# Optimization experiments

Hardware: AMD Instinct MI355X
Metric: run time of the kernel (lower is better)

The kernel has to match this reference:

```python
import jax, jax.numpy as jnp
import numpy as np

D = 1024      # hidden_size
FF = 4096     # ff_inner_dim = 4 * D
E = 8         # num_experts
K = 2         # moe_top_k
B, L = 4, 1024


def setup_inputs() -> dict:
    key = jax.random.key(0)
    ks = jax.random.split(key, 12)
    s = 0.02  # weight init scale
    return {
        "x": jax.random.normal(ks[0], (B, L, D), jnp.float32),
        "W_gate": jax.random.normal(ks[1], (D, E), jnp.float32) * s,
        "W1": jax.random.normal(ks[2], (E, D, FF), jnp.float32) * s,
        "b1": jnp.zeros((E, FF), jnp.float32),
        "W2": jax.random.normal(ks[3], (E, FF, D), jnp.float32) * s,
        "b2": jnp.zeros((E, D), jnp.float32),
        "Ws1": jax.random.normal(ks[4], (D, FF), jnp.float32) * s,
        "bs1": jnp.zeros((FF,), jnp.float32),
        "Ws2": jax.random.normal(ks[5], (FF, D), jnp.float32) * s,
        "bs2": jnp.zeros((D,), jnp.float32),
    }


def _gelu(h):
    # torch F.gelu default = exact (erf) gelu
    return jax.nn.gelu(h, approximate=False)


def reference(x, W_gate, W1, b1, W2, b2, Ws1, bs1, Ws2, bs2):
    Bx, Lx, Dx = x.shape
    xf = x.reshape(-1, Dx)                       # [T, D]
    logits = xf @ W_gate                         # [T, E]
    probs = jax.nn.softmax(logits, axis=-1)
    top_v, top_i = jax.lax.top_k(probs, K)       # [T, K]
    top_v = top_v / jnp.sum(top_v, axis=-1, keepdims=True)
    # dense combine weights: [T, E], zero for unselected experts
    combine = jnp.sum(jax.nn.one_hot(top_i, E, dtype=xf.dtype) * top_v[..., None], axis=1)

    out = jnp.zeros_like(xf)
    for e in range(E):  # fixed small expert loop, unrolled under jit
        h = _gelu(xf @ W1[e] + b1[e])            # [T, FF]
        out = out + combine[:, e:e + 1] * (h @ W2[e] + b2[e])

    shared = _gelu(xf @ Ws1 + bs1) @ Ws2 + bs2   # [T, D]
    return (out + shared).reshape(Bx, Lx, Dx)
```

## Files before the change

kernel.cpp:

```cpp
#include <hip/hip_runtime.h>
#include <hip/hip_bf16.h>

typedef unsigned short ushort_t;
typedef __attribute__((ext_vector_type(4))) float f32x4;
typedef __attribute__((ext_vector_type(8))) short bf16x8;
typedef __attribute__((ext_vector_type(8))) unsigned short us8;

#define T_TOK 4096
#define D_DIM 1024
#define FF_DIM 4096
#define NE 8
#define ESTRIDE 4194304L

__device__ __forceinline__ unsigned short f2bf(float f) {
  __hip_bfloat16 h = __float2bfloat16(f);
  return __builtin_bit_cast(unsigned short, h);
}
__device__ __forceinline__ float bf2f(ushort_t u) {
  unsigned int x = ((unsigned int)u) << 16;
  return __builtin_bit_cast(float, x);
}
__device__ __forceinline__ float gelu_f(float v) {
  return 0.5f * v * (1.0f + erff(v * 0.70710678118654752440f));
}

__global__ __launch_bounds__(256) void pre_kernel(
    const float* __restrict__ x, const float* __restrict__ Wg,
    const float* __restrict__ W1, const float* __restrict__ Ws1,
    int* __restrict__ cnt, int* __restrict__ tok,
    float* __restrict__ wof, int* __restrict__ rankof,
    ushort_t* __restrict__ Xbf, ushort_t* __restrict__ W1T) {
  __shared__ ushort_t tile[128][136];
  const int bid = blockIdx.x, tid = threadIdx.x;

  if (bid < 1024) {
    const int t = bid * 4 + (tid >> 6);
    const int lane = tid & 63;
    const float* xr = x + (long)t * D_DIM;
    ushort_t* xb = Xbf + (long)t * D_DIM;
    float acc[NE];
#pragma unroll
    for (int e = 0; e < NE; e++) acc[e] = 0.f;
#pragma unroll
    for (int i = 0; i < 16; i++) {
      int d = i * 64 + lane;
      float xv = xr[d];
      xb[d] = f2bf(xv);
      const float* wr = Wg + d * NE;
#pragma unroll
      for (int e = 0; e < NE; e++) acc[e] += xv * wr[e];
    }
#pragma unroll
    for (int off = 32; off > 0; off >>= 1) {
#pragma unroll
      for (int e = 0; e < NE; e++) acc[e] += __shfl_xor(acc[e], off, 64);
    }
    if (lane == 0) {
      int i0 = 0;
#pragma unroll
      for (int e = 1; e < NE; e++) if (acc[e] > acc[i0]) i0 = e;
      int i1 = -1;
#pragma unroll
      for (int e = 0; e < NE; e++) {
        if (e == i0) continue;
        if (i1 < 0 || acc[e] > acc[i1]) i1 = e;
      }
      float e1 = expf(acc[i1] - acc[i0]);
      float w0 = 1.f / (1.f + e1);
      float w1 = e1 * w0;
      int s0 = atomicAdd(&cnt[i0], 1);
      tok[i0 * T_TOK + s0] = t; wof[i0 * T_TOK + s0] = w0; rankof[i0 * T_TOK + s0] = 0;
      int s1 = atomicAdd(&cnt[i1], 1);
      tok[i1 * T_TOK + s1] = t; wof[i1 * T_TOK + s1] = w1; rankof[i1 * T_TOK + s1] = 1;
      tok[8 * T_TOK + t] = t; wof[8 * T_TOK + t] = 1.f; rankof[8 * T_TOK + t] = 0;
    }
    return;
  }

  int tix = bid - 1024;
  if (tix >= 2304) return;
  const int e = tix >> 8;
  const int rem = tix & 255;
  const int r0 = (rem >> 5) * 128, c0 = (rem & 31) * 128;
  const float* src = (e == 8) ? Ws1 : (W1 + (long)e * 4194304);
  ushort_t* d = W1T + (long)e * ESTRIDE;
#pragma unroll
  for (int i = 0; i < 16; i++) {
    int lin = tid + i * 256;
    int r = lin >> 5, c = (lin & 31) * 4;
    float4 v = *(const float4*)(src + (long)(r0 + r) * 4096 + c0 + c);
    tile[c + 0][r] = f2bf(v.x);
    tile[c + 1][r] = f2bf(v.y);
    tile[c + 2][r] = f2bf(v.z);
    tile[c + 3][r] = f2bf(v.w);
  }
  __syncthreads();
#pragma unroll
  for (int i = 0; i < 8; i++) {
    int lin = tid + i * 256;
    int cc = lin >> 4, rp = lin & 15;
    us8 v = *(const us8*)&tile[cc][rp * 8];
    *(us8*)(d + (long)(c0 + cc) * 1024 + r0 + rp * 8) = v;
  }
}

__global__ void build_queue_kernel(const int* __restrict__ cnt, int* __restrict__ base,
                                   unsigned int* __restrict__ q1,
                                   unsigned int* __restrict__ q2,
                                   int* __restrict__ nq, int* __restrict__ cnt8) {
  const int e = blockIdx.x;
  int off1 = 0, off2 = 0, tot1 = 0, tot2 = 0, M = 0;
  for (int i = 0; i < 9; i++) {
    int c = (i == 8) ? T_TOK : cnt[i];
    int m = (c + 255) >> 8;
    if (i < e) { off1 += m * 16; off2 += m * 4; }
    if (i == e) M = m;
    tot1 += m * 16; tot2 += m * 4;
  }
  for (int i = threadIdx.x; i < M * 16; i += 256) {
    int my = i >> 4, nx = i & 15;
    int ms = my >> 1, mi = my & 1, ns = nx >> 2, ni = nx & 3;
    int h = M - ms * 2; if (h > 2) h = 2;
    int pos = ms * 32 + ns * (h * 4) + mi * 4 + ni;
    q1[off1 + pos] = ((unsigned)e << 16) | ((unsigned)my << 8) | (unsigned)nx;
  }
  for (int i = threadIdx.x; i < M * 4; i += 256) {
    int my = i >> 2, nx = i & 3;
    int pos = nx * M + my;
    q2[off2 + pos] = ((unsigned)e << 16) | ((unsigned)my << 8) | (unsigned)nx;
  }
  if (e == 0 && threadIdx.x == 0) {
    nq[0] = tot1; nq[1] = tot2;
    int s = 0;
    for (int i = 0; i < NE; i++) { base[i] = s; s += cnt[i]; }
    base[8] = s;
    *cnt8 = T_TOK;
  }
}

template <int K, int N, int PHASE, bool FUSE>
__global__ __launch_bounds__(1024, 1) void gemm_kernel(
    const ushort_t* __restrict__ Abase, const ushort_t* __restrict__ WT,
    const float* __restrict__ bias_e, const float* __restrict__ bias_s,
    const int* __restrict__ cnt, const int* __restrict__ base,
    const int* __restrict__ tok, const float* __restrict__ wof,
    const int* __restrict__ rankof,
    const unsigned int* __restrict__ q, const int* __restrict__ nq_all,
    ushort_t* __restrict__ He, ushort_t* __restrict__ ybuf, float* __restrict__ out,
    const float* __restrict__ W2src, const float* __restrict__ Ws2src,
    ushort_t* __restrict__ W2Tdst) {
  __shared__ char smem[131072];
  const int tid = threadIdx.x;
  const int bid = blockIdx.x;
  const int NBLK = FUSE ? 1024 : (int)gridDim.x;

  if (FUSE && bid >= 1024) {
    int tix = bid - 1024;
    if (tix >= 2304) return;
    const int e = tix >> 8;
    const int rem = tix & 255;
    const int r0 = (rem >> 3) * 128, c0 = (rem & 7) * 128;
    const float* src = (e == 8) ? Ws2src : (W2src + (long)e * 4194304);
    ushort_t* d = W2Tdst + (long)e * ESTRIDE;
    ushort_t (*tile)[136] = (ushort_t (*)[136])smem;
#pragma unroll
    for (int i = 0; i < 4; i++) {
      int lin = tid + i * 1024;
      int r = lin >> 5, c = (lin & 31) * 4;
      float4 v = *(const float4*)(src + (long)(r0 + r) * 1024 + c0 + c);
      tile[c + 0][r] = f2bf(v.x);
      tile[c + 1][r] = f2bf(v.y);
      tile[c + 2][r] = f2bf(v.z);
      tile[c + 3][r] = f2bf(v.w);
    }
    __syncthreads();
#pragma unroll
    for (int i = 0; i < 2; i++) {
      int lin = tid + i * 1024;
      int cc = lin >> 4, rp = lin & 15;
      us8 v = *(const us8*)&tile[cc][rp * 8];
      *(us8*)(d + (long)(c0 + cc) * 4096 + r0 + rp * 8) = v;
    }
    return;
  }

  const int nq = nq_all[PHASE - 1];
  const int chunk = NBLK >> 3;
  const int vbid = (bid < (chunk << 3)) ? ((bid & 7) * chunk + (bid >> 3)) : bid;

  const int w = tid >> 6, lane = tid & 63;
  const int wm = w >> 2, wn = w & 3;
  const int lr = lane & 15, lg = lane >> 4;
  char* const lds = smem;

  const int srow = tid >> 2;
  const int cg = ((tid & 3) - (srow >> 1)) & 3;

  int offA[4], offB[4];
#pragma unroll
  for (int m = 0; m < 4; m++) {
    int r = wm * 64 + m * 16 + lr;
    offA[m] = r * 64 + (((lg + (r >> 1)) & 3) << 4);
  }
#pragma unroll
  for (int n = 0; n < 4; n++) {
    int r = wn * 64 + n * 16 + lr;
    offB[n] = r * 64 + (((lg + (r >> 1)) & 3) << 4);
  }

  constexpr int NT = K / 32;

#define STAGE(buf_, kk_)                                                        \
  do {                                                                          \
    char* dd_ = lds + (buf_) * 32768 + tid * 16;                                \
    __builtin_amdgcn_global_load_lds(                                           \
        (const __attribute__((address_space(1))) void*)(pA + (kk_)),            \
        (__attribute__((address_space(3))) void*)(dd_), 16, 0, 0);              \
    __builtin_amdgcn_global_load_lds(                                           \
        (const __attribute__((address_space(1))) void*)(pB + (kk_)),            \
        (__attribute__((address_space(3))) void*)(dd_ + 16384), 16, 0, 0);      \
  } while (0)

  for (int it = vbid; it < nq; it += NBLK) {
    const unsigned int item = q[it];
    const int e = item >> 16;
    const int m0 = ((item >> 8) & 0xff) * 256;
    const int n0 = (item & 0xff) * 256;
    const int count = cnt[e];

    int rr = m0 + srow;
    int rc = (rr < count) ? rr : 0;
    long arow;
    if (PHASE == 1) arow = tok[e * T_TOK + rc];
    else            arow = (long)base[e] + rc;
    const ushort_t* pA = Abase + arow * (long)K + cg * 8;
    const ushort_t* pB = WT + (long)e * ESTRIDE + (long)(n0 + srow) * K + cg * 8;

    f32x4 acc[4][4] = {};

    __builtin_amdgcn_s_barrier();
    asm volatile("" ::: "memory");
    STAGE(0, 0); STAGE(1, 32); STAGE(2, 64);

    for (int t = 0; t < NT; t++) {
      if (t + 3 < NT) {
        STAGE((t + 3) & 3, (t + 3) * 32);
        asm volatile("s_waitcnt vmcnt(6)" ::: "memory");
      } else if (t + 3 == NT) {
        asm volatile("s_waitcnt vmcnt(4)" ::: "memory");
      } else if (t + 2 == NT) {
        asm volatile("s_waitcnt vmcnt(2)" ::: "memory");
      } else {
        asm volatile("s_waitcnt vmcnt(0)" ::: "memory");
      }
      __builtin_amdgcn_s_barrier();
      asm volatile("" ::: "memory");

      const char* aB = lds + (t & 3) * 32768;
      const char* bB = aB + 16384;
      bf16x8 av[4], bv[4];
#pragma unroll
      for (int m = 0; m < 4; m++) av[m] = *(const bf16x8*)(aB + offA[m]);
#pragma unroll
      for (int n = 0; n < 4; n++) bv[n] = *(const bf16x8*)(bB + offB[n]);
#pragma unroll
      for (int m = 0; m < 4; m++)
#pragma unroll
        for (int n = 0; n < 4; n++)
          acc[m][n] = __builtin_amdgcn_mfma_f32_16x16x32_bf16(av[m], bv[n], acc[m][n], 0, 0, 0);

      __builtin_amdgcn_s_barrier();
      asm volatile("" ::: "memory");
    }

    const float* bias = (e == NE) ? bias_s : (bias_e + (long)e * N);
#pragma unroll
    for (int m = 0; m < 4; m++) {
#pragma unroll
      for (int j = 0; j < 4; j++) {
        int rloc = wm * 64 + m * 16 + lg * 4 + j;
        int rrr = m0 + rloc;
        if (rrr >= count) continue;
        if (PHASE == 1) {
          long orow = (long)base[e] + rrr;
#pragma unroll
          for (int n = 0; n < 4; n++) {
            int col = n0 + wn * 64 + n * 16 + lr;
            float v = acc[m][n][j] + bias[col];
            He[orow * FF_DIM + col] = f2bf(gelu_f(v));
          }
        } else {
          int tt = tok[e * T_TOK + rrr];
          if (e == NE) {
#pragma unroll
            for (int n = 0; n < 4; n++) {
              int col = n0 + wn * 64 + n * 16 + lr;
              out[(long)tt * D_DIM + col] = acc[m][n][j] + bias[col];
            }
          } else {
            float wgt = wof[e * T_TOK + rrr];
            int rk = rankof[e * T_TOK + rrr];
            ushort_t* dst = ybuf + (long)rk * ((long)T_TOK * D_DIM) + (long)tt * D_DIM;
#pragma unroll
            for (int n = 0; n < 4; n++) {
              int col = n0 + wn * 64 + n * 16 + lr;
              dst[col] = f2bf(wgt * (acc[m][n][j] + bias[col]));
            }
          }
        }
      }
    }
  }
#undef STAGE
}

__global__ void final_add_kernel(float* __restrict__ out, const ushort_t* __restrict__ ybuf) {
  long i = ((long)blockIdx.x * 256 + threadIdx.x) * 8;
  float4 a0 = *(const float4*)(out + i);
  float4 a1 = *(const float4*)(out + i + 4);
  us8 b = *(const us8*)(ybuf + i);
  us8 c = *(const us8*)(ybuf + (long)T_TOK * D_DIM + i);
  float r[8];
#pragma unroll
  for (int k = 0; k < 8; k++) r[k] = bf2f(b[k]) + bf2f(c[k]);
  a0.x += r[0]; a0.y += r[1]; a0.z += r[2]; a0.w += r[3];
  a1.x += r[4]; a1.y += r[5]; a1.z += r[6]; a1.w += r[7];
  *(float4*)(out + i) = a0;
  *(float4*)(out + i + 4) = a1;
}

extern "C" void kernel_launch(void* const* d_in, const int* in_sizes, int n_in,
                              void* d_out, int out_size, void* d_ws, size_t ws_size,
                              hipStream_t stream) {
  (void)in_sizes; (void)n_in; (void)out_size; (void)ws_size;
  const float* x   = (const float*)d_in[0];
  const float* Wg  = (const float*)d_in[1];
  const float* W1  = (const float*)d_in[2];
  const float* b1  = (const float*)d_in[3];
  const float* W2  = (const float*)d_in[4];
  const float* b2  = (const float*)d_in[5];
  const float* Ws1 = (const float*)d_in[6];
  const float* bs1 = (const float*)d_in[7];
  const float* Ws2 = (const float*)d_in[8];
  const float* bs2 = (const float*)d_in[9];
  float* out = (float*)d_out;

  char* ws = (char*)d_ws;
  int*      cnt    = (int*)(ws + 0);
  int*      base   = (int*)(ws + 64);
  int*      tok    = (int*)(ws + 256);
  float*    wof    = (float*)(ws + 256 + 147456);
  int*      rankof = (int*)(ws + 256 + 2 * 147456);
  ushort_t* Xbf    = (ushort_t*)(ws + 442624);
  ushort_t* W1T    = (ushort_t*)(ws + 8831232);
  ushort_t* W2T    = (ushort_t*)(ws + 84328704);
  ushort_t* He     = (ushort_t*)(ws + 159826176);
  int*      nq     = (int*)(ws + 260489472);
  unsigned int* q1 = (unsigned int*)(ws + 260489536);
  unsigned int* q2 = (unsigned int*)(ws + 260489536 + 32768);
  ushort_t* ybuf   = (ushort_t*)(ws + 261538048);

  hipMemsetAsync(cnt, 0, 64, stream);
  pre_kernel<<<3328, 256, 0, stream>>>(x, Wg, W1, Ws1, cnt, tok, wof, rankof, Xbf, W1T);
  build_queue_kernel<<<9, 256, 0, stream>>>(cnt, base, q1, q2, nq, &cnt[8]);
  gemm_kernel<1024, 4096, 1, true><<<3328, 1024, 0, stream>>>(
      Xbf, W1T, b1, bs1, cnt, base, tok, wof, rankof, q1, nq, He, ybuf, out,
      W2, Ws2, W2T);
  gemm_kernel<4096, 1024, 2, false><<<256, 1024, 0, stream>>>(
      He, W2T, b2, bs2, cnt, base, tok, wof, rankof, q2, nq, He, ybuf, out,
      nullptr, nullptr, nullptr);
  final_add_kernel<<<2048, 256, 0, stream>>>(out, ybuf);
}
```

Measured before the change: 507.2 us.

## Use double-buffered LDS staging and fp32 expert output buffer

The GEMM mainloop goes from a 4-stage LDS ring with three tiles in flight to a 2-stage double buffer with one tile prefetched, halving shared memory to 64KB. The per-rank expert output buffer changes from bf16 to fp32, and the final add kernel reads fp32 directly. Shallower prefetch exposes more global memory latency in the mainloop. The fp32 buffer doubles the memory traffic for the expert outputs but improves accuracy.

```diff
diff --git a/kernel.cpp b/kernel.cpp
--- a/kernel.cpp
+++ b/kernel.cpp
@@ -15,10 +15,6 @@
 __device__ __forceinline__ unsigned short f2bf(float f) {
   __hip_bfloat16 h = __float2bfloat16(f);
   return __builtin_bit_cast(unsigned short, h);
-}
-__device__ __forceinline__ float bf2f(ushort_t u) {
-  unsigned int x = ((unsigned int)u) << 16;
-  return __builtin_bit_cast(float, x);
 }
 __device__ __forceinline__ float gelu_f(float v) {
   return 0.5f * v * (1.0f + erff(v * 0.70710678118654752440f));
@@ -146,10 +142,10 @@
     const int* __restrict__ tok, const float* __restrict__ wof,
     const int* __restrict__ rankof,
     const unsigned int* __restrict__ q, const int* __restrict__ nq_all,
-    ushort_t* __restrict__ He, ushort_t* __restrict__ ybuf, float* __restrict__ out,
+    ushort_t* __restrict__ He, float* __restrict__ ybuf, float* __restrict__ out,
     const float* __restrict__ W2src, const float* __restrict__ Ws2src,
     ushort_t* __restrict__ W2Tdst) {
-  __shared__ char smem[131072];
+  __shared__ char smem[65536];
   const int tid = threadIdx.x;
   const int bid = blockIdx.x;
   const int NBLK = FUSE ? 1024 : (int)gridDim.x;
@@ -240,15 +236,11 @@
 
     __builtin_amdgcn_s_barrier();
     asm volatile("" ::: "memory");
-    STAGE(0, 0); STAGE(1, 32); STAGE(2, 64);
+    STAGE(0, 0);
 
     for (int t = 0; t < NT; t++) {
-      if (t + 3 < NT) {
-        STAGE((t + 3) & 3, (t + 3) * 32);
-        asm volatile("s_waitcnt vmcnt(6)" ::: "memory");
-      } else if (t + 3 == NT) {
-        asm volatile("s_waitcnt vmcnt(4)" ::: "memory");
-      } else if (t + 2 == NT) {
+      if (t + 1 < NT) {
+        STAGE((t + 1) & 1, (t + 1) * 32);
         asm volatile("s_waitcnt vmcnt(2)" ::: "memory");
       } else {
         asm volatile("s_waitcnt vmcnt(0)" ::: "memory");
@@ -256,7 +248,7 @@
       __builtin_amdgcn_s_barrier();
       asm volatile("" ::: "memory");
 
-      const char* aB = lds + (t & 3) * 32768;
+      const char* aB = lds + (t & 1) * 32768;
       const char* bB = aB + 16384;
       bf16x8 av[4], bv[4];
 #pragma unroll
@@ -300,11 +292,11 @@
           } else {
             float wgt = wof[e * T_TOK + rrr];
             int rk = rankof[e * T_TOK + rrr];
-            ushort_t* dst = ybuf + (long)rk * ((long)T_TOK * D_DIM) + (long)tt * D_DIM;
+            float* dst = ybuf + (long)rk * ((long)T_TOK * D_DIM) + (long)tt * D_DIM;
 #pragma unroll
             for (int n = 0; n < 4; n++) {
               int col = n0 + wn * 64 + n * 16 + lr;
-              dst[col] = f2bf(wgt * (acc[m][n][j] + bias[col]));
+              dst[col] = wgt * (acc[m][n][j] + bias[col]);
             }
           }
         }
@@ -314,19 +306,13 @@
 #undef STAGE
 }
 
-__global__ void final_add_kernel(float* __restrict__ out, const ushort_t* __restrict__ ybuf) {
-  long i = ((long)blockIdx.x * 256 + threadIdx.x) * 8;
-  float4 a0 = *(const float4*)(out + i);
-  float4 a1 = *(const float4*)(out + i + 4);
-  us8 b = *(const us8*)(ybuf + i);
-  us8 c = *(const us8*)(ybuf + (long)T_TOK * D_DIM + i);
-  float r[8];
-#pragma unroll
-  for (int k = 0; k < 8; k++) r[k] = bf2f(b[k]) + bf2f(c[k]);
-  a0.x += r[0]; a0.y += r[1]; a0.z += r[2]; a0.w += r[3];
-  a1.x += r[4]; a1.y += r[5]; a1.z += r[6]; a1.w += r[7];
-  *(float4*)(out + i) = a0;
-  *(float4*)(out + i + 4) = a1;
+__global__ void final_add_kernel(float* __restrict__ out, const float* __restrict__ ybuf) {
+  long i = ((long)blockIdx.x * 256 + threadIdx.x) * 4;
+  float4 a = *(const float4*)(out + i);
+  float4 b = *(const float4*)(ybuf + i);
+  float4 c = *(const float4*)(ybuf + (long)T_TOK * D_DIM + i);
+  a.x += b.x + c.x; a.y += b.y + c.y; a.z += b.z + c.z; a.w += b.w + c.w;
+  *(float4*)(out + i) = a;
 }
 
 extern "C" void kernel_launch(void* const* d_in, const int* in_sizes, int n_in,
@@ -358,7 +344,7 @@
   int*      nq     = (int*)(ws + 260489472);
   unsigned int* q1 = (unsigned int*)(ws + 260489536);
   unsigned int* q2 = (unsigned int*)(ws + 260489536 + 32768);
-  ushort_t* ybuf   = (ushort_t*)(ws + 261538048);
+  float*    ybuf   = (float*)(ws + 261538048);
 
   hipMemsetAsync(cnt, 0, 64, stream);
   pre_kernel<<<3328, 256, 0, stream>>>(x, Wg, W1, Ws1, cnt, tok, wof, rankof, Xbf, W1T);
@@ -369,5 +355,5 @@
   gemm_kernel<4096, 1024, 2, false><<<256, 1024, 0, stream>>>(
       He, W2T, b2, bs2, cnt, base, tok, wof, rankof, q2, nq, He, ybuf, out,
       nullptr, nullptr, nullptr);
-  final_add_kernel<<<2048, 256, 0, stream>>>(out, ybuf);
-}
+  final_add_kernel<<<4096, 256, 0, stream>>>(out, ybuf);
+}
```

Measured after the change: 507.7 us. About the same (+0.1%).
